# Kernel tuning notes

Measured on AMD Instinct MI355X. Metric: run time of the kernel, lower is better.

The kernel has to match this reference:

```python
import jax, jax.numpy as jnp
import numpy as np

DELTA = 16
L_S = 32
HID = 8      # fast SSM hidden dim
GH = 64      # slow GRU hidden
OD = 2 * HID # slow branch output dim


def setup_inputs() -> dict:
    key = jax.random.key(0)
    ks = jax.random.split(key, 9)
    B, T = 128, 65536
    x = jax.random.normal(ks[0], (B, T), dtype=jnp.float32)
    # fast branch params: f_in: Linear(1, HID, bias=False); f_out: Linear(HID, 1, bias=False)
    w_in = jax.random.normal(ks[1], (HID,), dtype=jnp.float32) * 0.3
    w_out = jax.random.normal(ks[2], (HID,), dtype=jnp.float32) * 0.3
    # slow branch GRU (input_size=1) + output linear
    w_ih = jax.random.normal(ks[3], (3 * GH,), dtype=jnp.float32) * 0.1
    w_hh = jax.random.normal(ks[4], (3 * GH, GH), dtype=jnp.float32) * 0.1
    b_ih = jax.random.normal(ks[5], (3 * GH,), dtype=jnp.float32) * 0.1
    b_hh = jax.random.normal(ks[6], (3 * GH,), dtype=jnp.float32) * 0.1
    w_sl = jax.random.normal(ks[7], (OD, GH), dtype=jnp.float32) * 0.1
    b_sl = jax.random.normal(ks[8], (OD,), dtype=jnp.float32) * 0.1
    return {"x": x, "w_in": w_in, "w_out": w_out, "w_ih": w_ih, "w_hh": w_hh,
            "b_ih": b_ih, "b_hh": b_hh, "w_sl": w_sl, "b_sl": b_sl}


def _slow_branch(frames, w_ih, w_hh, b_ih, b_hh, w_sl, b_sl):
    # frames: (B, F, L_S). GRU over the L_S samples of each frame, last hidden -> Linear.
    B, F, L = frames.shape
    seq = frames.reshape(B * F, L).T  # (L, B*F), time-major

    def gru_step(h, xt):
        gi = xt[:, None] * w_ih[None, :] + b_ih          # (N, 3GH)
        gh = h @ w_hh.T + b_hh                            # (N, 3GH)
        ir, iz, inn = jnp.split(gi, 3, axis=-1)
        hr, hz, hn = jnp.split(gh, 3, axis=-1)
        r = jax.nn.sigmoid(ir + hr)
        z = jax.nn.sigmoid(iz + hz)
        n = jnp.tanh(inn + r * hn)
        h = (1.0 - z) * n + z * h
        return h, None

    h0 = jnp.zeros((B * F, GH), dtype=frames.dtype)
    hT, _ = jax.lax.scan(gru_step, h0, seq)
    eps = hT @ w_sl.T + b_sl                              # (B*F, OD)
    return eps.reshape(B, F, OD)


def reference(x, w_in, w_out, w_ih, w_hh, b_ih, b_hh, w_sl, b_sl):
    B, T = x.shape
    F = (T - L_S) // DELTA + 1
    # x.unfold(1, 32, delta) -> gather frames (B, F, L_S)
    idx = jnp.arange(F)[:, None] * DELTA + jnp.arange(L_S)[None, :]
    frames = x[:, idx]                                    # (B, F, L_S)
    eps = _slow_branch(frames, w_ih, w_hh, b_ih, b_hh, w_sl, b_sl)
    A_s = jax.nn.sigmoid(eps[..., :HID])                  # (B, F, H)
    g_s = eps[..., HID:]                                  # (B, F, H)
    # per-timestep frame index j = clamp(i // delta - 1, 0)
    j = jnp.clip(jnp.arange(T) // DELTA - 1, 0, F - 1)
    A_t = A_s[:, j]                                       # (B, T, H)
    g_t = g_s[:, j]                                       # (B, T, H)
    # x_emb = f_in(x) * g  (f_in has no bias)
    u_t = x[:, :, None] * w_in[None, None, :] * g_t       # (B, T, H)

    def step(h, inp):
        A, u = inp
        h = A * h + u
        return h, h

    h0 = jnp.zeros((B, HID), dtype=x.dtype)
    _, hs = jax.lax.scan(step, h0, (A_t.transpose(1, 0, 2), u_t.transpose(1, 0, 2)))  # hs: (T, B, H)
    y = jnp.einsum('tbh,h->bt', hs, w_out)                # f_out, no bias
    return y
```

## Files before the change

kernel.cpp:

```cpp
#include <hip/hip_runtime.h>
#include <hip/hip_bf16.h>
#include <math.h>

#define B_SZ 128
#define T_SZ 65536
#define F_FR 4095
#define GHID 64
#define HID 8
#define CHUNK 256
#define NCH (T_SZ / CHUNK)

typedef _Float16 half8 __attribute__((ext_vector_type(8)));
typedef float f32x4 __attribute__((ext_vector_type(4)));

#define L2E 1.4426950408889634f

static __device__ __forceinline__ float frcp(float v) {
#if __has_builtin(__builtin_amdgcn_rcpf)
    return __builtin_amdgcn_rcpf(v);
#else
    return 1.0f / v;
#endif
}
static __device__ __forceinline__ float fexp2(float v) {
#if __has_builtin(__builtin_amdgcn_exp2f)
    return __builtin_amdgcn_exp2f(v);
#else
    return exp2f(v);
#endif
}
__device__ __forceinline__ float sigm(float xv) { return frcp(1.0f + fexp2(-L2E * xv)); }

#define FSTR 68
#define XSTR 34

__global__ __launch_bounds__(256) __attribute__((amdgpu_waves_per_eu(2, 2)))
void gru_mfma(
    const float* __restrict__ x, const float* __restrict__ w_ih,
    const float* __restrict__ w_hh, const float* __restrict__ b_ih,
    const float* __restrict__ b_hh, const float* __restrict__ w_sl,
    const float* __restrict__ b_sl, float* __restrict__ ag)
{
    __shared__ _Float16 wlds[24 * 64 * 8];
    __shared__ float hx[4][32 * FSTR + 32 * XSTR];
    const int tid  = threadIdx.x;
    const int wv   = tid >> 6;
    const int lane = tid & 63;
    const int c16  = lane & 15;
    const int g    = lane >> 4;
    float* hb = &hx[wv][0];
    float* xs = hb + 32 * FSTR;
    const int tile = ((int)blockIdx.x * 4 + wv) * 32;

#pragma unroll
    for (int f = 0; f < 24; f += 4) {
        const int fi = f + wv;
        const int n = fi >> 1, c = fi & 1;
        const float sc = (n < 8) ? -L2E : (2.0f * L2E);
        const float* wp = w_hh + (16 * n + c16) * 64 + 32 * c + 8 * g;
        const float4 q0 = *(const float4*)wp;
        const float4 q1 = *(const float4*)(wp + 4);
        half8 w8;
        w8[0] = (_Float16)(sc * q0.x); w8[1] = (_Float16)(sc * q0.y);
        w8[2] = (_Float16)(sc * q0.z); w8[3] = (_Float16)(sc * q0.w);
        w8[4] = (_Float16)(sc * q1.x); w8[5] = (_Float16)(sc * q1.y);
        w8[6] = (_Float16)(sc * q1.z); w8[7] = (_Float16)(sc * q1.w);
        *(half8*)(wlds + (fi * 64 + lane) * 8) = w8;
    }

    float wiR[4], wiZ[4], wiN[4], bR[4], bZ[4], biN[4], bhN[4];
#pragma unroll
    for (int m = 0; m < 4; ++m) {
        const int j = c16 + 16 * m;
        wiR[m] = -L2E * w_ih[j];
        wiZ[m] = -L2E * w_ih[64 + j];
        wiN[m] = 2.0f * L2E * w_ih[128 + j];
        bR[m]  = -L2E * (b_ih[j] + b_hh[j]);
        bZ[m]  = -L2E * (b_ih[64 + j] + b_hh[64 + j]);
        biN[m] = 2.0f * L2E * b_ih[128 + j];
        bhN[m] = 2.0f * L2E * b_hh[128 + j];
    }

    {
        const int sl = lane & 31, half = lane >> 5;
        const int s = tile + sl;
        const int b = s / F_FR;
        const int f = s % F_FR;
        const float* xp = x + (long)b * T_SZ + f * 16 + 16 * half;
        const float4 p0 = *(const float4*)xp;
        const float4 p1 = *(const float4*)(xp + 4);
        const float4 p2 = *(const float4*)(xp + 8);
        const float4 p3 = *(const float4*)(xp + 12);
        float* xd = xs + sl * XSTR + 16 * half;
        *(float4*)(xd)      = p0;  *(float4*)(xd + 4)  = p1;
        *(float4*)(xd + 8)  = p2;  *(float4*)(xd + 12) = p3;
    }
    for (int idx = lane; idx < 32 * FSTR; idx += 64) hb[idx] = 0.0f;
    __syncthreads();

    const f32x4 zz = {0.0f, 0.0f, 0.0f, 0.0f};
    float ho[2][4][4];
#pragma unroll
    for (int mt = 0; mt < 2; ++mt)
#pragma unroll
        for (int m = 0; m < 4; ++m)
#pragma unroll
            for (int r = 0; r < 4; ++r) ho[mt][m][r] = 0.0f;

#pragma unroll 1
    for (int t = 0; t < 32; ++t) {
        half8 ah[2][2], al[2][2];
#pragma unroll
        for (int mt = 0; mt < 2; ++mt)
#pragma unroll
        for (int c = 0; c < 2; ++c) {
            const float* rp = hb + (c16 + 16 * mt) * FSTR + 32 * c + 8 * g;
            const float4 u0 = *(const float4*)rp;
            const float4 u1 = *(const float4*)(rp + 4);
            const float fv[8] = {u0.x, u0.y, u0.z, u0.w, u1.x, u1.y, u1.z, u1.w};
#pragma unroll
            for (int e = 0; e < 8; ++e) {
                const _Float16 hi = (_Float16)fv[e];
                ah[mt][c][e] = hi;
                al[mt][c][e] = (_Float16)(fv[e] - (float)hi);
            }
        }

        f32x4 acc[2][12];
#pragma unroll
        for (int n = 0; n < 12; ++n) {
            const half8 b0 = *(const half8*)(wlds + ((2 * n + 0) * 64 + lane) * 8);
            const half8 b1 = *(const half8*)(wlds + ((2 * n + 1) * 64 + lane) * 8);
#pragma unroll
            for (int mt = 0; mt < 2; ++mt) {
                f32x4 a = __builtin_amdgcn_mfma_f32_16x16x32_f16(ah[mt][0], b0, zz, 0, 0, 0);
                a = __builtin_amdgcn_mfma_f32_16x16x32_f16(al[mt][0], b0, a, 0, 0, 0);
                a = __builtin_amdgcn_mfma_f32_16x16x32_f16(ah[mt][1], b1, a, 0, 0, 0);
                acc[mt][n] = __builtin_amdgcn_mfma_f32_16x16x32_f16(al[mt][1], b1, a, 0, 0, 0);
            }
        }

#pragma unroll
        for (int mt = 0; mt < 2; ++mt) {
            float xt4[4];
#pragma unroll
            for (int r = 0; r < 4; ++r) xt4[r] = xs[(4 * g + r + 16 * mt) * XSTR + t];
#pragma unroll
            for (int m = 0; m < 4; ++m) {
                const int jm = c16 + 16 * m;
#pragma unroll
                for (int r = 0; r < 4; ++r) {
                    const float uR = fmaf(xt4[r], wiR[m], bR[m]) + acc[mt][m][r];
                    const float rr = frcp(1.0f + fexp2(uR));
                    const float uZ = fmaf(xt4[r], wiZ[m], bZ[m]) + acc[mt][4 + m][r];
                    const float zf = frcp(1.0f + fexp2(uZ));
                    const float uN = fmaf(rr, acc[mt][8 + m][r] + bhN[m],
                                          fmaf(xt4[r], wiN[m], biN[m]));
                    const float nn = fmaf(-2.0f, frcp(1.0f + fexp2(uN)), 1.0f);
                    const float hnew = fmaf(zf, ho[mt][m][r] - nn, nn);
                    ho[mt][m][r] = hnew;
                    hb[(4 * g + r + 16 * mt) * FSTR + jm] = hnew;
                }
            }
        }
    }

    half8 wsl[2];
#pragma unroll
    for (int c = 0; c < 2; ++c) {
        const float4 q0 = *(const float4*)(w_sl + c16 * 64 + 32 * c + 8 * g);
        const float4 q1 = *(const float4*)(w_sl + c16 * 64 + 32 * c + 8 * g + 4);
        wsl[c][0] = (_Float16)q0.x; wsl[c][1] = (_Float16)q0.y;
        wsl[c][2] = (_Float16)q0.z; wsl[c][3] = (_Float16)q0.w;
        wsl[c][4] = (_Float16)q1.x; wsl[c][5] = (_Float16)q1.y;
        wsl[c][6] = (_Float16)q1.z; wsl[c][7] = (_Float16)q1.w;
    }
    const float bs = b_sl[c16];
#pragma unroll
    for (int mt = 0; mt < 2; ++mt) {
        half8 fh[2], fl[2];
#pragma unroll
        for (int c = 0; c < 2; ++c) {
            const float* rp = hb + (c16 + 16 * mt) * FSTR + 32 * c + 8 * g;
            const float4 u0 = *(const float4*)rp;
            const float4 u1 = *(const float4*)(rp + 4);
            const float fv[8] = {u0.x, u0.y, u0.z, u0.w, u1.x, u1.y, u1.z, u1.w};
#pragma unroll
            for (int e = 0; e < 8; ++e) {
                const _Float16 hi = (_Float16)fv[e];
                fh[c][e] = hi;
                fl[c][e] = (_Float16)(fv[e] - (float)hi);
            }
        }
        f32x4 ec = __builtin_amdgcn_mfma_f32_16x16x32_f16(fh[0], wsl[0], zz, 0, 0, 0);
        ec = __builtin_amdgcn_mfma_f32_16x16x32_f16(fl[0], wsl[0], ec, 0, 0, 0);
        ec = __builtin_amdgcn_mfma_f32_16x16x32_f16(fh[1], wsl[1], ec, 0, 0, 0);
        ec = __builtin_amdgcn_mfma_f32_16x16x32_f16(fl[1], wsl[1], ec, 0, 0, 0);
#pragma unroll
        for (int r = 0; r < 4; ++r) {
            float e = ec[r] + bs;
            if (c16 < 8) e = sigm(e);
            ag[(long)(tile + 16 * mt + 4 * g + r) * 16 + c16] = e;
        }
    }
}

__global__ __launch_bounds__(256) void fast_chunk(
    const float* __restrict__ x, const float* __restrict__ ag,
    const float* __restrict__ w_in,
    float* __restrict__ chP, float* __restrict__ chH)
{
    const int tid = blockIdx.x * 256 + threadIdx.x;
    const int b = tid / NCH, c = tid % NCH;
    float h[HID], P[HID];
#pragma unroll
    for (int i = 0; i < HID; ++i) { h[i] = 0.0f; P[i] = 1.0f; }
    const float* xp = x + (long)b * T_SZ + c * CHUNK;

#pragma unroll 1
    for (int g = 0; g < CHUNK / 16; ++g) {
        const int t0 = c * CHUNK + g * 16;
        int fr = t0 / 16 - 1; fr = max(0, min(F_FR - 1, fr));
        const float4* agp = (const float4*)(ag + ((long)b * F_FR + fr) * 16);
        const float4 a0 = agp[0], a1 = agp[1], g0 = agp[2], g1 = agp[3];
        const float A[HID]  = {a0.x, a0.y, a0.z, a0.w, a1.x, a1.y, a1.z, a1.w};
        const float Gv[HID] = {g0.x, g0.y, g0.z, g0.w, g1.x, g1.y, g1.z, g1.w};
        float wg[HID];
#pragma unroll
        for (int i = 0; i < HID; ++i) wg[i] = w_in[i] * Gv[i];
#pragma unroll
        for (int tt = 0; tt < 16; ++tt) {
            const float xt = xp[g * 16 + tt];
#pragma unroll
            for (int i = 0; i < HID; ++i) h[i] = fmaf(A[i], h[i], xt * wg[i]);
        }
#pragma unroll
        for (int i = 0; i < HID; ++i) {
            const float a2 = A[i] * A[i]; const float a4 = a2 * a2; const float a8 = a4 * a4;
            P[i] *= a8 * a8;
        }
    }
    float* pp = chP + (long)tid * HID;
    float* hp = chH + (long)tid * HID;
#pragma unroll
    for (int i = 0; i < HID; ++i) { pp[i] = P[i]; hp[i] = h[i]; }
}

__global__ __launch_bounds__(256) void chunk_scan(
    const float* __restrict__ chP, const float* __restrict__ chH,
    float* __restrict__ st)
{
    const int tid = blockIdx.x * 256 + threadIdx.x;
    if (tid >= B_SZ * HID) return;
    const int b = tid / HID, i = tid % HID;
    float h = 0.0f;
#pragma unroll 1
    for (int c = 0; c < NCH; ++c) {
        const long idx = ((long)b * NCH + c) * HID + i;
        st[idx] = h;
        h = fmaf(chP[idx], h, chH[idx]);
    }
}

__global__ __launch_bounds__(256) void fast_apply(
    const float* __restrict__ x, const float* __restrict__ ag,
    const float* __restrict__ w_in, const float* __restrict__ w_out,
    const float* __restrict__ st, float* __restrict__ y)
{
    const int tid = blockIdx.x * 256 + threadIdx.x;
    const int b = tid / NCH, c = tid % NCH;
    float h[HID];
    const float* sp = st + (long)tid * HID;
#pragma unroll
    for (int i = 0; i < HID; ++i) h[i] = sp[i];
    float wo[HID];
#pragma unroll
    for (int i = 0; i < HID; ++i) wo[i] = w_out[i];
    const float* xp = x + (long)b * T_SZ + c * CHUNK;
    float* yp = y + (long)b * T_SZ + c * CHUNK;

#pragma unroll 1
    for (int g = 0; g < CHUNK / 16; ++g) {
        const int t0 = c * CHUNK + g * 16;
        int fr = t0 / 16 - 1; fr = max(0, min(F_FR - 1, fr));
        const float4* agp = (const float4*)(ag + ((long)b * F_FR + fr) * 16);
        const float4 a0 = agp[0], a1 = agp[1], g0 = agp[2], g1 = agp[3];
        const float A[HID]  = {a0.x, a0.y, a0.z, a0.w, a1.x, a1.y, a1.z, a1.w};
        const float Gv[HID] = {g0.x, g0.y, g0.z, g0.w, g1.x, g1.y, g1.z, g1.w};
        float wg[HID];
#pragma unroll
        for (int i = 0; i < HID; ++i) wg[i] = w_in[i] * Gv[i];
#pragma unroll
        for (int tt = 0; tt < 16; ++tt) {
            const float xt = xp[g * 16 + tt];
            float acc = 0.0f;
#pragma unroll
            for (int i = 0; i < HID; ++i) {
                h[i] = fmaf(A[i], h[i], xt * wg[i]);
                acc = fmaf(h[i], wo[i], acc);
            }
            yp[g * 16 + tt] = acc;
        }
    }
}

extern "C" void kernel_launch(void* const* d_in, const int* in_sizes, int n_in,
                              void* d_out, int out_size, void* d_ws, size_t ws_size,
                              hipStream_t stream) {
    const float* x    = (const float*)d_in[0];
    const float* w_in = (const float*)d_in[1];
    const float* w_out= (const float*)d_in[2];
    const float* w_ih = (const float*)d_in[3];
    const float* w_hh = (const float*)d_in[4];
    const float* b_ih = (const float*)d_in[5];
    const float* b_hh = (const float*)d_in[6];
    const float* w_sl = (const float*)d_in[7];
    const float* b_sl = (const float*)d_in[8];
    float* y = (float*)d_out;

    float* ag  = (float*)d_ws;
    size_t off = (size_t)B_SZ * F_FR * 16;
    float* chP = ag + off;
    float* chH = chP + (size_t)B_SZ * NCH * HID;
    float* st  = chH + (size_t)B_SZ * NCH * HID;

    gru_mfma<<<4095, 256, 0, stream>>>(x, w_ih, w_hh, b_ih, b_hh, w_sl, b_sl, ag);
    fast_chunk<<<(B_SZ * NCH) / 256, 256, 0, stream>>>(x, ag, w_in, chP, chH);
    chunk_scan<<<(B_SZ * HID + 255) / 256, 256, 0, stream>>>(chP, chH, st);
    fast_apply<<<(B_SZ * NCH) / 256, 256, 0, stream>>>(x, ag, w_in, w_out, st, y);
}
```

Measured before the change: 1.363 ms.

## Interleave GRU gate MFMAs with activation per hidden slice, seed bias in accumulator

Restructures the per-timestep GRU loop so the R/Z/N gate MFMAs for each 16-column hidden slice are computed and then consumed by the activation math right away, instead of computing all 24 accumulators first. This shrinks live accumulator registers (from 96 floats to 24) and lets the compiler overlap MFMA with transcendental work. It also seeds the accumulators with the hidden biases to drop separate adds, and removes the fixed waves_per_eu(2,2) hint so occupancy follows register use. The accumulation order changes slightly, and occupancy is no longer pinned.

```diff
diff --git a/kernel.cpp b/kernel.cpp
--- a/kernel.cpp
+++ b/kernel.cpp
@@ -34,7 +34,7 @@
 #define FSTR 68
 #define XSTR 34
 
-__global__ __launch_bounds__(256) __attribute__((amdgpu_waves_per_eu(2, 2)))
+__global__ __launch_bounds__(256)
 void gru_mfma(
     const float* __restrict__ x, const float* __restrict__ w_ih,
     const float* __restrict__ w_hh, const float* __restrict__ b_ih,
@@ -98,7 +98,6 @@
     for (int idx = lane; idx < 32 * FSTR; idx += 64) hb[idx] = 0.0f;
     __syncthreads();
 
-    const f32x4 zz = {0.0f, 0.0f, 0.0f, 0.0f};
     float ho[2][4][4];
 #pragma unroll
     for (int mt = 0; mt < 2; ++mt)
@@ -125,37 +124,46 @@
                 al[mt][c][e] = (_Float16)(fv[e] - (float)hi);
             }
         }
-
-        f32x4 acc[2][12];
-#pragma unroll
-        for (int n = 0; n < 12; ++n) {
-            const half8 b0 = *(const half8*)(wlds + ((2 * n + 0) * 64 + lane) * 8);
-            const half8 b1 = *(const half8*)(wlds + ((2 * n + 1) * 64 + lane) * 8);
+        float xt4[2][4];
+#pragma unroll
+        for (int mt = 0; mt < 2; ++mt)
+#pragma unroll
+        for (int r = 0; r < 4; ++r) xt4[mt][r] = xs[(4 * g + r + 16 * mt) * XSTR + t];
+
+#pragma unroll
+        for (int m = 0; m < 4; ++m) {
+            f32x4 aR[2], aZ[2], aN[2];
 #pragma unroll
             for (int mt = 0; mt < 2; ++mt) {
-                f32x4 a = __builtin_amdgcn_mfma_f32_16x16x32_f16(ah[mt][0], b0, zz, 0, 0, 0);
-                a = __builtin_amdgcn_mfma_f32_16x16x32_f16(al[mt][0], b0, a, 0, 0, 0);
-                a = __builtin_amdgcn_mfma_f32_16x16x32_f16(ah[mt][1], b1, a, 0, 0, 0);
-                acc[mt][n] = __builtin_amdgcn_mfma_f32_16x16x32_f16(al[mt][1], b1, a, 0, 0, 0);
-            }
-        }
-
-#pragma unroll
-        for (int mt = 0; mt < 2; ++mt) {
-            float xt4[4];
-#pragma unroll
-            for (int r = 0; r < 4; ++r) xt4[r] = xs[(4 * g + r + 16 * mt) * XSTR + t];
-#pragma unroll
-            for (int m = 0; m < 4; ++m) {
-                const int jm = c16 + 16 * m;
+                aR[mt] = f32x4{bR[m], bR[m], bR[m], bR[m]};
+                aZ[mt] = f32x4{bZ[m], bZ[m], bZ[m], bZ[m]};
+                aN[mt] = f32x4{bhN[m], bhN[m], bhN[m], bhN[m]};
+            }
+#pragma unroll
+            for (int c = 0; c < 2; ++c) {
+                const half8 bfR = *(const half8*)(wlds + ((2 * m + c)       * 64 + lane) * 8);
+                const half8 bfZ = *(const half8*)(wlds + ((2 * (4 + m) + c) * 64 + lane) * 8);
+                const half8 bfN = *(const half8*)(wlds + ((2 * (8 + m) + c) * 64 + lane) * 8);
+#pragma unroll
+                for (int mt = 0; mt < 2; ++mt) {
+                    aR[mt] = __builtin_amdgcn_mfma_f32_16x16x32_f16(ah[mt][c], bfR, aR[mt], 0, 0, 0);
+                    aR[mt] = __builtin_amdgcn_mfma_f32_16x16x32_f16(al[mt][c], bfR, aR[mt], 0, 0, 0);
+                    aZ[mt] = __builtin_amdgcn_mfma_f32_16x16x32_f16(ah[mt][c], bfZ, aZ[mt], 0, 0, 0);
+                    aZ[mt] = __builtin_amdgcn_mfma_f32_16x16x32_f16(al[mt][c], bfZ, aZ[mt], 0, 0, 0);
+                    aN[mt] = __builtin_amdgcn_mfma_f32_16x16x32_f16(ah[mt][c], bfN, aN[mt], 0, 0, 0);
+                    aN[mt] = __builtin_amdgcn_mfma_f32_16x16x32_f16(al[mt][c], bfN, aN[mt], 0, 0, 0);
+                }
+            }
+            const int jm = c16 + 16 * m;
+#pragma unroll
+            for (int mt = 0; mt < 2; ++mt) {
 #pragma unroll
                 for (int r = 0; r < 4; ++r) {
-                    const float uR = fmaf(xt4[r], wiR[m], bR[m]) + acc[mt][m][r];
+                    const float uR = fmaf(xt4[mt][r], wiR[m], aR[mt][r]);
                     const float rr = frcp(1.0f + fexp2(uR));
-                    const float uZ = fmaf(xt4[r], wiZ[m], bZ[m]) + acc[mt][4 + m][r];
+                    const float uZ = fmaf(xt4[mt][r], wiZ[m], aZ[mt][r]);
                     const float zf = frcp(1.0f + fexp2(uZ));
-                    const float uN = fmaf(rr, acc[mt][8 + m][r] + bhN[m],
-                                          fmaf(xt4[r], wiN[m], biN[m]));
+                    const float uN = fmaf(rr, aN[mt][r], fmaf(xt4[mt][r], wiN[m], biN[m]));
                     const float nn = fmaf(-2.0f, frcp(1.0f + fexp2(uN)), 1.0f);
                     const float hnew = fmaf(zf, ho[mt][m][r] - nn, nn);
                     ho[mt][m][r] = hnew;
@@ -165,6 +173,7 @@
         }
     }
 
+    const f32x4 zz = {0.0f, 0.0f, 0.0f, 0.0f};
     half8 wsl[2];
 #pragma unroll
     for (int c = 0; c < 2; ++c) {
```

New measurement: 1.410 ms. +3.5%, slower.
